# Kernel optimization log

Measured on AMD Instinct MI355X. Metric: run time of the kernel, lower is better.

Reference implementation:

```python
import jax, jax.numpy as jnp
import numpy as np

NUM_HEADS = 8
QUERY_DIM = 512
VALUE_DIM = 512
INPUT_DIM = 512
Q_HEAD = QUERY_DIM // NUM_HEADS   # 64
V_HEAD = VALUE_DIM // NUM_HEADS   # 64
TOPK = 5
BN_EPS = 1e-5


def setup_inputs() -> dict:
    key = jax.random.key(0)
    ks = jax.random.split(key, 3)
    B = 2048
    x = jax.random.normal(ks[0], (B, INPUT_DIM), dtype=jnp.float32)
    # small init scale so softmax logits are reasonable
    W_qkv = jax.random.normal(ks[1], (INPUT_DIM, 2 * QUERY_DIM + VALUE_DIM), dtype=jnp.float32) * 0.02
    W_proj = jax.random.normal(ks[2], (VALUE_DIM, VALUE_DIM), dtype=jnp.float32) * 0.02
    b_proj = jnp.zeros((VALUE_DIM,), dtype=jnp.float32)
    bn_gamma = jnp.ones((VALUE_DIM,), dtype=jnp.float32)
    bn_beta = jnp.zeros((VALUE_DIM,), dtype=jnp.float32)
    return {"x": x, "W_qkv": W_qkv, "W_proj": W_proj, "b_proj": b_proj,
            "bn_gamma": bn_gamma, "bn_beta": bn_beta}


def _batchnorm_train(y, gamma, beta):
    # torch BatchNorm1d training mode: batch mean, biased variance
    mean = y.mean(axis=0)
    var = y.var(axis=0)  # biased (ddof=0), matches torch normalization
    return gamma * (y - mean) * jax.lax.rsqrt(var + BN_EPS) + beta


def reference(x, W_qkv, W_proj, b_proj, bn_gamma, bn_beta):
    B = x.shape[0]
    # qkv_transform: Linear(input_dim, 2Q + V, bias=False)
    qkv = x @ W_qkv                                   # [B, 2Q+V]
    qv = qkv[:, :2 * QUERY_DIM].reshape(B, 2, NUM_HEADS, Q_HEAD)
    q = qv[:, 0].transpose(1, 0, 2)                   # [H, B, hd]
    k = qv[:, 1].transpose(1, 0, 2)                   # [H, B, hd]
    v = qkv[:, 2 * QUERY_DIM:].reshape(B, NUM_HEADS, V_HEAD).transpose(1, 0, 2)  # [H, B, vd]

    scale = 1.0 / jnp.sqrt(jnp.float32(Q_HEAD))
    logits = jnp.einsum('hqd,hkd->hqk', q, k) * scale  # [H, B, B]
    attn = jax.nn.softmax(logits, axis=-1)

    # per-head: zero the top-5 columns by summed attention weight (no grad through selection)
    col_sums = jax.lax.stop_gradient(attn.sum(axis=1))           # [H, B]
    _, top_idx = jax.lax.top_k(col_sums, TOPK)                   # [H, 5]
    mask = jnp.ones((NUM_HEADS, B), dtype=attn.dtype)
    mask = mask.at[jnp.arange(NUM_HEADS)[:, None], top_idx].set(0.0)
    attn = attn * mask[:, None, :]                               # zero columns

    out = jnp.einsum('hqk,hkd->hqd', attn, v)                    # [H, B, vd]
    out = out.transpose(1, 0, 2).reshape(B, VALUE_DIM)
    # proj: Linear + BatchNorm1d (training mode) + ReLU
    out = out @ W_proj.T + b_proj
    out = jax.nn.relu(_batchnorm_train(out, bn_gamma, bn_beta))
    return out, attn
```

## Files before the change

### kernel.cpp

```cpp
#include <hip/hip_runtime.h>
#include <hip/hip_bf16.h>

#define B 2048
#define NH 8
#define HD 64
#define DIM 512
#define QKVN 1536
#define OUT0_ELEMS ((size_t)B * DIM)

typedef float f32x4 __attribute__((ext_vector_type(4)));
typedef __bf16 bf16x8 __attribute__((ext_vector_type(8)));

static __device__ __forceinline__ unsigned short f2bf(float f) {
    unsigned int u = __builtin_bit_cast(unsigned int, f);
    u += 0x7fffu + ((u >> 16) & 1u);
    return (unsigned short)(u >> 16);
}
static __device__ __forceinline__ float bfhi2f(unsigned int u) {
    return __builtin_bit_cast(float, u & 0xffff0000u);
}
static __device__ __forceinline__ float bflo2f(unsigned int u) {
    return __builtin_bit_cast(float, u << 16);
}

__global__ __launch_bounds__(256) void prep_cast(const float* __restrict__ x,
                                                 const float* __restrict__ wp,
                                                 const float* __restrict__ wqkv,
                                                 unsigned short* __restrict__ xbf,
                                                 unsigned short* __restrict__ wpbf,
                                                 unsigned short* __restrict__ wT,
                                                 float* __restrict__ zero_region) {
    int bx = blockIdx.x;
    int tid = threadIdx.x;
    if (bx < 1280) {
        size_t t = (size_t)bx * 256 + tid;
        const float4* src;
        ushort4* dst;
        size_t idx;
        if (t < 262144) { src = (const float4*)x; dst = (ushort4*)xbf; idx = t; }
        else            { src = (const float4*)wp; dst = (ushort4*)wpbf; idx = t - 262144; }
        float4 v = src[idx];
        ushort4 u;
        u.x = f2bf(v.x); u.y = f2bf(v.y); u.z = f2bf(v.z); u.w = f2bf(v.w);
        dst[idx] = u;
        return;
    }
    if (bx >= 1472) {
        int idx = (bx - 1472) * 256 + tid;
        if (idx < 8448)
            ((float4*)zero_region)[idx] = make_float4(0.f, 0.f, 0.f, 0.f);
        return;
    }
    int b = bx - 1280;
    int n0 = (b % 24) * 64;
    int k0 = (b / 24) * 64;
    __shared__ unsigned short T[64][72];
#pragma unroll
    for (int it = 0; it < 4; ++it) {
        int chunk = it * 256 + tid;
        int r = chunk >> 4, c4 = (chunk & 15) * 4;
        float4 v = *(const float4*)(wqkv + (size_t)(k0 + r) * QKVN + n0 + c4);
        T[c4 + 0][r] = f2bf(v.x); T[c4 + 1][r] = f2bf(v.y);
        T[c4 + 2][r] = f2bf(v.z); T[c4 + 3][r] = f2bf(v.w);
    }
    __syncthreads();
#pragma unroll
    for (int it = 0; it < 2; ++it) {
        int chunk = it * 256 + tid;
        int r = chunk >> 3, c8 = (chunk & 7) * 8;
        ushort4 u0, u1;
        u0.x = T[r][c8 + 0]; u0.y = T[r][c8 + 1]; u0.z = T[r][c8 + 2]; u0.w = T[r][c8 + 3];
        u1.x = T[r][c8 + 4]; u1.y = T[r][c8 + 5]; u1.z = T[r][c8 + 6]; u1.w = T[r][c8 + 7];
        *(ushort4*)(wT + (size_t)(n0 + r) * 512 + k0 + c8) = u0;
        *(ushort4*)(wT + (size_t)(n0 + r) * 512 + k0 + c8 + 4) = u1;
    }
}

__global__ __launch_bounds__(256) void gemm_qkv_mfma(const unsigned short* __restrict__ xbf,
                                                     const unsigned short* __restrict__ wT,
                                                     float* __restrict__ v_f32,
                                                     unsigned short* __restrict__ qkbf,
                                                     unsigned short* __restrict__ vT) {
    int nt = blockIdx.x;
    int mt = blockIdx.y;
    __shared__ uint4 Ax[128 * 8];
    __shared__ uint4 Bw[64 * 8];
    int tid = threadIdx.x;
    int l = tid & 63, wid = tid >> 6;
    int wr = wid >> 1, wc = wid & 1;
    const uint4* x4 = (const uint4*)xbf;
    const uint4* w4 = (const uint4*)wT;
    f32x4 acc[4][2];
#pragma unroll
    for (int i = 0; i < 4; ++i)
#pragma unroll
        for (int j = 0; j < 2; ++j) acc[i][j] = (f32x4){0.f, 0.f, 0.f, 0.f};

    for (int kt = 0; kt < 8; ++kt) {
        int kg = kt * 8;
#pragma unroll
        for (int it = 0; it < 4; ++it) {
            int chunk = it * 256 + tid;
            int row = chunk >> 3, slot = chunk & 7;
            Ax[row * 8 + (slot ^ (row & 7))] = x4[(size_t)(mt * 128 + row) * 64 + kg + slot];
        }
#pragma unroll
        for (int it = 0; it < 2; ++it) {
            int chunk = it * 256 + tid;
            int row = chunk >> 3, slot = chunk & 7;
            Bw[row * 8 + (slot ^ (row & 7))] = w4[(size_t)(nt * 64 + row) * 64 + kg + slot];
        }
        __syncthreads();
#pragma unroll
        for (int km = 0; km < 2; ++km) {
            int gsel = km * 4 + (l >> 4);
            bf16x8 a[4], b[2];
#pragma unroll
            for (int i = 0; i < 4; ++i) {
                int row = wr * 64 + i * 16 + (l & 15);
                a[i] = __builtin_bit_cast(bf16x8, Ax[row * 8 + (gsel ^ (row & 7))]);
            }
#pragma unroll
            for (int j = 0; j < 2; ++j) {
                int row = wc * 32 + j * 16 + (l & 15);
                b[j] = __builtin_bit_cast(bf16x8, Bw[row * 8 + (gsel ^ (row & 7))]);
            }
#pragma unroll
            for (int i = 0; i < 4; ++i)
#pragma unroll
                for (int j = 0; j < 2; ++j)
                    acc[i][j] = __builtin_amdgcn_mfma_f32_16x16x32_bf16(a[i], b[j], acc[i][j], 0, 0, 0);
        }
        __syncthreads();
    }
    if (nt < 16) {
        float qscale = (nt < 8) ? 0.125f : 1.0f;
#pragma unroll
        for (int i = 0; i < 4; ++i)
#pragma unroll
            for (int j = 0; j < 2; ++j)
#pragma unroll
                for (int reg = 0; reg < 4; ++reg) {
                    int row = mt * 128 + wr * 64 + i * 16 + (l >> 4) * 4 + reg;
                    int col = nt * 64 + wc * 32 + j * 16 + (l & 15);
                    qkbf[(size_t)row * 1024 + col] = f2bf(acc[i][j][reg] * qscale);
                }
    } else {
        int h = nt - 16;
#pragma unroll
        for (int i = 0; i < 4; ++i)
#pragma unroll
            for (int j = 0; j < 2; ++j) {
                int k0r = mt * 128 + wr * 64 + i * 16 + (l >> 4) * 4;
                int d = wc * 32 + j * 16 + (l & 15);
                uint2 pk;
                pk.x = (unsigned)f2bf(acc[i][j][0]) | ((unsigned)f2bf(acc[i][j][1]) << 16);
                pk.y = (unsigned)f2bf(acc[i][j][2]) | ((unsigned)f2bf(acc[i][j][3]) << 16);
                *(uint2*)(vT + ((size_t)(h * 64 + d) * 2048 + k0r)) = pk;
#pragma unroll
                for (int reg = 0; reg < 4; ++reg)
                    v_f32[(size_t)(k0r + reg) * DIM + h * 64 + d] = acc[i][j][reg];
            }
    }
}

template<int PHASE>
__global__ __launch_bounds__(256) void attn_pass(const unsigned short* __restrict__ qkbf,
                                                 const unsigned short* __restrict__ vT,
                                                 const float* __restrict__ rowsum_in,
                                                 float* __restrict__ rowsum_out,
                                                 float* __restrict__ attn,
                                                 float* __restrict__ colsum,
                                                 float* __restrict__ ovp) {
    int ct = blockIdx.x, qt = blockIdx.y, h = blockIdx.z;
    int tid = threadIdx.x;
    int l = tid & 63;
    int wid = tid >> 6;
    int wr = wid >> 1;
    int wc = wid & 1;

    __shared__ uint4 Qs[128 * 8];
    __shared__ uint4 Ks[64 * 8];
    __shared__ uint4 Vt[64 * 8];
    __shared__ uint4 Pl4[128 * 8];
    __shared__ float cs[512];
    __shared__ float rinv[128];
    unsigned short* Pl = (unsigned short*)Pl4;

    const uint4* src = (const uint4*)qkbf;
#pragma unroll
    for (int it = 0; it < 4; ++it) {
        int chunk = it * 256 + tid;
        int row = chunk >> 3, slot = chunk & 7;
        Qs[row * 8 + (slot ^ (row & 7))] = src[(size_t)(qt * 128 + row) * 128 + h * 8 + slot];
    }
    if constexpr (PHASE == 2) {
        if (tid < 128) rinv[tid] = 1.0f / rowsum_in[h * B + qt * 128 + tid];
        if (tid < 256) { cs[tid] = 0.f; cs[tid + 256] = 0.f; }
    }

    float rsum[4][4];
    f32x4 O[4][2];
    if constexpr (PHASE == 1) {
#pragma unroll
        for (int i = 0; i < 4; ++i)
#pragma unroll
            for (int r = 0; r < 4; ++r) rsum[i][r] = 0.f;
    } else {
#pragma unroll
        for (int i = 0; i < 4; ++i)
#pragma unroll
            for (int j = 0; j < 2; ++j) O[i][j] = (f32x4){0.f, 0.f, 0.f, 0.f};
    }

    size_t hbb = (size_t)h * B * B;
    for (int sub = 0; sub < 8; ++sub) {
        int kbase = ct * 512 + sub * 64;
#pragma unroll
        for (int it = 0; it < 2; ++it) {
            int chunk = it * 256 + tid;
            int row = chunk >> 3, slot = chunk & 7;
            Ks[row * 8 + (slot ^ (row & 7))] = src[(size_t)(kbase + row) * 128 + 64 + h * 8 + slot];
        }
        if constexpr (PHASE == 2) {
#pragma unroll
            for (int it = 0; it < 2; ++it) {
                int chunk = it * 256 + tid;
                int d = chunk >> 3, g = chunk & 7;
                Vt[d * 8 + (g ^ (d & 7))] =
                    *(const uint4*)(vT + ((size_t)(h * 64 + d) * 2048 + kbase + g * 8));
            }
        }
        __syncthreads();

        f32x4 S[4][2];
#pragma unroll
        for (int i = 0; i < 4; ++i)
#pragma unroll
            for (int j = 0; j < 2; ++j) S[i][j] = (f32x4){0.f, 0.f, 0.f, 0.f};
#pragma unroll
        for (int km = 0; km < 2; ++km) {
            int gsel = km * 4 + (l >> 4);
            bf16x8 aq[4], bk[2];
#pragma unroll
            for (int i = 0; i < 4; ++i) {
                int row = wr * 64 + i * 16 + (l & 15);
                aq[i] = __builtin_bit_cast(bf16x8, Qs[row * 8 + (gsel ^ (row & 7))]);
            }
#pragma unroll
            for (int j = 0; j < 2; ++j) {
                int row = wc * 32 + j * 16 + (l & 15);
                bk[j] = __builtin_bit_cast(bf16x8, Ks[row * 8 + (gsel ^ (row & 7))]);
            }
#pragma unroll
            for (int i = 0; i < 4; ++i)
#pragma unroll
                for (int j = 0; j < 2; ++j)
                    S[i][j] = __builtin_amdgcn_mfma_f32_16x16x32_bf16(aq[i], bk[j], S[i][j], 0, 0, 0);
        }

        if constexpr (PHASE == 1) {
#pragma unroll
            for (int i = 0; i < 4; ++i)
#pragma unroll
                for (int j = 0; j < 2; ++j)
#pragma unroll
                    for (int reg = 0; reg < 4; ++reg)
                        rsum[i][reg] += __expf(S[i][j][reg]);
            __syncthreads();
        } else {
            float csacc[2] = {0.f, 0.f};
#pragma unroll
            for (int i = 0; i < 4; ++i) {
#pragma unroll
                for (int j = 0; j < 2; ++j) {
                    int kcol = wc * 32 + j * 16 + (l & 15);
#pragma unroll
                    for (int reg = 0; reg < 4; ++reg) {
                        int qrow = wr * 64 + i * 16 + (l >> 4) * 4 + reg;
                        float p = __expf(S[i][j][reg]) * rinv[qrow];
                        csacc[j] += p;
                        Pl[qrow * 64 + ((kcol & 7) | ((((kcol >> 3) ^ (qrow & 7))) << 3))] = f2bf(p);
                    }
                }
            }
#pragma unroll
            for (int j = 0; j < 2; ++j) {
                float v = csacc[j];
                v += __shfl_xor(v, 16);
                v += __shfl_xor(v, 32);
                if (l < 16) atomicAdd(&cs[sub * 64 + wc * 32 + j * 16 + l], v);
            }
            __syncthreads();
#pragma unroll
            for (int it2 = 0; it2 < 4; ++it2) {
                int chunk = it2 * 256 + tid;
                int row = chunk >> 3, g = chunk & 7;
                uint4 pv = Pl4[row * 8 + (g ^ (row & 7))];
                float4 lo, hi;
                lo.x = bflo2f(pv.x); lo.y = bfhi2f(pv.x);
                lo.z = bflo2f(pv.y); lo.w = bfhi2f(pv.y);
                hi.x = bflo2f(pv.z); hi.y = bfhi2f(pv.z);
                hi.z = bflo2f(pv.w); hi.w = bfhi2f(pv.w);
                float* dst = attn + hbb + (size_t)(qt * 128 + row) * B + kbase + g * 8;
                *(float4*)dst = lo;
                *(float4*)(dst + 4) = hi;
            }
#pragma unroll
            for (int km = 0; km < 2; ++km) {
                int gsel = km * 4 + (l >> 4);
                bf16x8 pa[4], vb[2];
#pragma unroll
                for (int i = 0; i < 4; ++i) {
                    int q = wr * 64 + i * 16 + (l & 15);
                    pa[i] = __builtin_bit_cast(bf16x8, Pl4[q * 8 + (gsel ^ (q & 7))]);
                }
#pragma unroll
                for (int j = 0; j < 2; ++j) {
                    int d = wc * 32 + j * 16 + (l & 15);
                    vb[j] = __builtin_bit_cast(bf16x8, Vt[d * 8 + (gsel ^ (d & 7))]);
                }
#pragma unroll
                for (int i = 0; i < 4; ++i)
#pragma unroll
                    for (int j = 0; j < 2; ++j)
                        O[i][j] = __builtin_amdgcn_mfma_f32_16x16x32_bf16(pa[i], vb[j], O[i][j], 0, 0, 0);
            }
            __syncthreads();
        }
    }

    if constexpr (PHASE == 1) {
#pragma unroll
        for (int i = 0; i < 4; ++i)
#pragma unroll
            for (int reg = 0; reg < 4; ++reg) {
                float v = rsum[i][reg];
                v += __shfl_xor(v, 1); v += __shfl_xor(v, 2);
                v += __shfl_xor(v, 4); v += __shfl_xor(v, 8);
                if ((l & 15) == 0)
                    atomicAdd(&rowsum_out[h * B + qt * 128 + wr * 64 + i * 16 + (l >> 4) * 4 + reg], v);
            }
    } else {
        for (int i = tid; i < 512; i += 256)
            atomicAdd(&colsum[h * B + ct * 512 + i], cs[i]);
#pragma unroll
        for (int i = 0; i < 4; ++i)
#pragma unroll
            for (int j = 0; j < 2; ++j)
#pragma unroll
                for (int reg = 0; reg < 4; ++reg) {
                    int qrow = wr * 64 + i * 16 + (l >> 4) * 4 + reg;
                    ovp[((size_t)ct * B + qt * 128 + qrow) * DIM + h * 64 + wc * 32 + j * 16 + (l & 15)] =
                        O[i][j][reg];
                }
    }
}

__global__ __launch_bounds__(256) void maskfix_topk(float* __restrict__ attn,
                                                    const float* __restrict__ v_f32,
                                                    const float* __restrict__ colsum,
                                                    const float* __restrict__ ovp,
                                                    unsigned short* __restrict__ ovbf) {
    int rt = blockIdx.x;
    int h = blockIdx.y;
    int tid = threadIdx.x;
    __shared__ float v[B];
    __shared__ float bv[256];
    __shared__ int bi[256];
    __shared__ float Pl[5][64];
    __shared__ float Vl[5][64];
    __shared__ int tix[5];
    for (int i = tid; i < B; i += 256) v[i] = colsum[h * B + i];
    __syncthreads();
    for (int it = 0; it < 5; ++it) {
        float best = -1e30f;
        int bidx = 0;
        for (int i = tid; i < B; i += 256) {
            float x = v[i];
            if (x > best || (x == best && i < bidx)) { best = x; bidx = i; }
        }
        bv[tid] = best; bi[tid] = bidx;
        __syncthreads();
        for (int s = 128; s > 0; s >>= 1) {
            if (tid < s) {
                if (bv[tid + s] > bv[tid] ||
                    (bv[tid + s] == bv[tid] && bi[tid + s] < bi[tid])) {
                    bv[tid] = bv[tid + s]; bi[tid] = bi[tid + s];
                }
            }
            __syncthreads();
        }
        if (tid == 0) { tix[it] = bi[0]; v[bi[0]] = -1e30f; }
        __syncthreads();
    }
    size_t abase = (size_t)h * B * B + (size_t)(rt * 64) * B;
    for (int t = tid; t < 320; t += 256) {
        int i = t / 64, q = t % 64;
        Pl[i][q] = attn[abase + (size_t)q * B + tix[i]];
        Vl[i][q] = v_f32[(size_t)tix[i] * DIM + h * 64 + q];
    }
    __syncthreads();
    for (int t = tid; t < 320; t += 256) {
        int i = t / 64, q = t % 64;
        attn[abase + (size_t)q * B + tix[i]] = 0.f;
    }
    int tx = tid % 16, ty = tid / 16;
    float corr[4][4] = {};
#pragma unroll
    for (int i = 0; i < 5; ++i)
#pragma unroll
        for (int a = 0; a < 4; ++a)
#pragma unroll
            for (int b2 = 0; b2 < 4; ++b2)
                corr[a][b2] += Pl[i][ty * 4 + a] * Vl[i][tx * 4 + b2];
#pragma unroll
    for (int a = 0; a < 4; ++a) {
        size_t row = (size_t)(rt * 64 + ty * 4 + a);
        size_t col = h * 64 + tx * 4;
        float4 s0 = *(const float4*)(ovp + ((size_t)0 * B + row) * DIM + col);
        float4 s1 = *(const float4*)(ovp + ((size_t)1 * B + row) * DIM + col);
        float4 s2 = *(const float4*)(ovp + ((size_t)2 * B + row) * DIM + col);
        float4 s3 = *(const float4*)(ovp + ((size_t)3 * B + row) * DIM + col);
        ushort4 u;
        u.x = f2bf(s0.x + s1.x + s2.x + s3.x - corr[a][0]);
        u.y = f2bf(s0.y + s1.y + s2.y + s3.y - corr[a][1]);
        u.z = f2bf(s0.z + s1.z + s2.z + s3.z - corr[a][2]);
        u.w = f2bf(s0.w + s1.w + s2.w + s3.w - corr[a][3]);
        *(ushort4*)(ovbf + row * DIM + col) = u;
    }
}

__global__ __launch_bounds__(256) void proj_gemm_mfma(const unsigned short* __restrict__ ovbf,
                                                      const unsigned short* __restrict__ wpbf,
                                                      const float* __restrict__ bproj,
                                                      float* __restrict__ y,
                                                      float* __restrict__ sums,
                                                      float* __restrict__ ssums) {
    int nt = blockIdx.x;
    int mt = blockIdx.y;
    __shared__ uint4 Ax[128 * 8];
    __shared__ uint4 Bw[64 * 8];
    __shared__ float sb[64];
    __shared__ float qb[64];
    int tid = threadIdx.x;
    int l = tid & 63, wid = tid >> 6;
    int wr = wid >> 1, wc = wid & 1;
    if (tid < 64) { sb[tid] = 0.f; qb[tid] = 0.f; }
    const uint4* a4 = (const uint4*)ovbf;
    const uint4* b4 = (const uint4*)wpbf;
    f32x4 acc[4][2];
#pragma unroll
    for (int i = 0; i < 4; ++i)
#pragma unroll
        for (int j = 0; j < 2; ++j) acc[i][j] = (f32x4){0.f, 0.f, 0.f, 0.f};

    for (int kt = 0; kt < 8; ++kt) {
        int kg = kt * 8;
#pragma unroll
        for (int it = 0; it < 4; ++it) {
            int chunk = it * 256 + tid;
            int row = chunk >> 3, slot = chunk & 7;
            Ax[row * 8 + (slot ^ (row & 7))] = a4[(size_t)(mt * 128 + row) * 64 + kg + slot];
        }
#pragma unroll
        for (int it = 0; it < 2; ++it) {
            int chunk = it * 256 + tid;
            int row = chunk >> 3, slot = chunk & 7;
            Bw[row * 8 + (slot ^ (row & 7))] = b4[(size_t)(nt * 64 + row) * 64 + kg + slot];
        }
        __syncthreads();
#pragma unroll
        for (int km = 0; km < 2; ++km) {
            int gsel = km * 4 + (l >> 4);
            bf16x8 a[4], b[2];
#pragma unroll
            for (int i = 0; i < 4; ++i) {
                int row = wr * 64 + i * 16 + (l & 15);
                a[i] = __builtin_bit_cast(bf16x8, Ax[row * 8 + (gsel ^ (row & 7))]);
            }
#pragma unroll
            for (int j = 0; j < 2; ++j) {
                int row = wc * 32 + j * 16 + (l & 15);
                b[j] = __builtin_bit_cast(bf16x8, Bw[row * 8 + (gsel ^ (row & 7))]);
            }
#pragma unroll
            for (int i = 0; i < 4; ++i)
#pragma unroll
                for (int j = 0; j < 2; ++j)
                    acc[i][j] = __builtin_amdgcn_mfma_f32_16x16x32_bf16(a[i], b[j], acc[i][j], 0, 0, 0);
        }
        __syncthreads();
    }
    float ls[2] = {0.f, 0.f};
    float lq[2] = {0.f, 0.f};
#pragma unroll
    for (int i = 0; i < 4; ++i)
#pragma unroll
        for (int j = 0; j < 2; ++j) {
            int col = nt * 64 + wc * 32 + j * 16 + (l & 15);
            float bp = bproj[col];
#pragma unroll
            for (int reg = 0; reg < 4; ++reg) {
                int row = mt * 128 + wr * 64 + i * 16 + (l >> 4) * 4 + reg;
                float c = acc[i][j][reg] + bp;
                y[(size_t)row * DIM + col] = c;
                ls[j] += c; lq[j] += c * c;
            }
        }
#pragma unroll
    for (int j = 0; j < 2; ++j) {
        atomicAdd(&sb[wc * 32 + j * 16 + (l & 15)], ls[j]);
        atomicAdd(&qb[wc * 32 + j * 16 + (l & 15)], lq[j]);
    }
    __syncthreads();
    if (tid < 64) {
        atomicAdd(&sums[nt * 64 + tid], sb[tid]);
        atomicAdd(&ssums[nt * 64 + tid], qb[tid]);
    }
}

__global__ __launch_bounds__(256) void bn_apply(const float* __restrict__ y,
                                                const float* __restrict__ sums,
                                                const float* __restrict__ ssums,
                                                const float* __restrict__ gamma,
                                                const float* __restrict__ beta,
                                                float* __restrict__ out) {
    int t = blockIdx.x * 256 + threadIdx.x;
    int c4 = (t % 128) * 4;
    size_t r = t / 128;
    if (r >= B) return;
    float4 s = *(const float4*)(sums + c4);
    float4 q = *(const float4*)(ssums + c4);
    float4 m, rs;
    m.x = s.x * (1.0f / B); m.y = s.y * (1.0f / B);
    m.z = s.z * (1.0f / B); m.w = s.w * (1.0f / B);
    rs.x = rsqrtf(q.x * (1.0f / B) - m.x * m.x + 1e-5f);
    rs.y = rsqrtf(q.y * (1.0f / B) - m.y * m.y + 1e-5f);
    rs.z = rsqrtf(q.z * (1.0f / B) - m.z * m.z + 1e-5f);
    rs.w = rsqrtf(q.w * (1.0f / B) - m.w * m.w + 1e-5f);
    float4 v = *(const float4*)(y + r * DIM + c4);
    float4 g = *(const float4*)(gamma + c4);
    float4 bt = *(const float4*)(beta + c4);
    float4 o;
    o.x = fmaxf(0.f, g.x * (v.x - m.x) * rs.x + bt.x);
    o.y = fmaxf(0.f, g.y * (v.y - m.y) * rs.y + bt.y);
    o.z = fmaxf(0.f, g.z * (v.z - m.z) * rs.z + bt.z);
    o.w = fmaxf(0.f, g.w * (v.w - m.w) * rs.w + bt.w);
    *(float4*)(out + r * DIM + c4) = o;
}

extern "C" void kernel_launch(void* const* d_in, const int* in_sizes, int n_in,
                              void* d_out, int out_size, void* d_ws, size_t ws_size,
                              hipStream_t stream) {
    const float* x = (const float*)d_in[0];
    const float* W_qkv = (const float*)d_in[1];
    const float* W_proj = (const float*)d_in[2];
    const float* b_proj = (const float*)d_in[3];
    const float* bn_gamma = (const float*)d_in[4];
    const float* bn_beta = (const float*)d_in[5];

    float* out0 = (float*)d_out;
    float* attn = (float*)d_out + OUT0_ELEMS;

    float* ws = (float*)d_ws;
    float* v_f32 = ws;
    float* ovp = v_f32 + OUT0_ELEMS;
    float* y = ovp + 4 * OUT0_ELEMS;
    float* rowsum = y + OUT0_ELEMS;
    float* colsum = rowsum + NH * B;
    float* sums = colsum + NH * B;
    float* ssums = sums + DIM;
    unsigned short* qkbf = (unsigned short*)(ssums + DIM);
    unsigned short* vT = qkbf + (size_t)B * 1024;
    unsigned short* wpbf = vT + (size_t)NH * HD * B;
    unsigned short* ovbf = wpbf + (size_t)DIM * DIM;
    unsigned short* xbf = (unsigned short*)ovp;
    unsigned short* wT = xbf + (size_t)B * 512;

    prep_cast<<<1280 + 192 + 33, 256, 0, stream>>>(x, W_proj, W_qkv, xbf, wpbf, wT, rowsum);
    gemm_qkv_mfma<<<dim3(QKVN / 64, B / 128), 256, 0, stream>>>(xbf, wT, v_f32, qkbf, vT);
    attn_pass<1><<<dim3(4, 16, NH), 256, 0, stream>>>(qkbf, vT, nullptr, rowsum,
                                                      attn, colsum, ovp);
    attn_pass<2><<<dim3(4, 16, NH), 256, 0, stream>>>(qkbf, vT, rowsum, nullptr,
                                                      attn, colsum, ovp);
    maskfix_topk<<<dim3(B / 64, NH), 256, 0, stream>>>(attn, v_f32, colsum, ovp, ovbf);
    proj_gemm_mfma<<<dim3(DIM / 64, B / 128), 256, 0, stream>>>(ovbf, wpbf, b_proj,
                                                                y, sums, ssums);
    bn_apply<<<(B * DIM / 4 + 255) / 256, 256, 0, stream>>>(y, sums, ssums,
                                                            bn_gamma, bn_beta, out0);
}
```

Measured before the change: 99.64 us.

## Fuse projection GEMM with batchnorm apply via grid-wide atomic barrier

Merges the projection GEMM and the batchnorm+ReLU kernel into one launch. All 128 blocks spin on a global atomic counter until every block has added its column sums, then normalize straight from the accumulator registers. This drops the y intermediate's write and re-read and one launch. It relies on all 128 blocks being co-resident, and the spin loop has a bounded timeout that could give wrong results if that does not hold.

```diff
diff --git a/kernel.cpp b/kernel.cpp
--- a/kernel.cpp
+++ b/kernel.cpp
@@ -47,7 +47,7 @@
     }
     if (bx >= 1472) {
         int idx = (bx - 1472) * 256 + tid;
-        if (idx < 8448)
+        if (idx < 8449)
             ((float4*)zero_region)[idx] = make_float4(0.f, 0.f, 0.f, 0.f);
         return;
     }
@@ -431,12 +431,15 @@
     }
 }
 
-__global__ __launch_bounds__(256) void proj_gemm_mfma(const unsigned short* __restrict__ ovbf,
-                                                      const unsigned short* __restrict__ wpbf,
-                                                      const float* __restrict__ bproj,
-                                                      float* __restrict__ y,
-                                                      float* __restrict__ sums,
-                                                      float* __restrict__ ssums) {
+__global__ __launch_bounds__(256) void proj_bn_fused(const unsigned short* __restrict__ ovbf,
+                                                     const unsigned short* __restrict__ wpbf,
+                                                     const float* __restrict__ bproj,
+                                                     const float* __restrict__ gamma,
+                                                     const float* __restrict__ beta,
+                                                     float* __restrict__ sums,
+                                                     float* __restrict__ ssums,
+                                                     int* __restrict__ ctr,
+                                                     float* __restrict__ out0) {
     int nt = blockIdx.x;
     int mt = blockIdx.y;
     __shared__ uint4 Ax[128 * 8];
@@ -495,19 +498,18 @@
     float ls[2] = {0.f, 0.f};
     float lq[2] = {0.f, 0.f};
 #pragma unroll
-    for (int i = 0; i < 4; ++i)
-#pragma unroll
-        for (int j = 0; j < 2; ++j) {
-            int col = nt * 64 + wc * 32 + j * 16 + (l & 15);
-            float bp = bproj[col];
+    for (int j = 0; j < 2; ++j) {
+        int col = nt * 64 + wc * 32 + j * 16 + (l & 15);
+        float bp = bproj[col];
+#pragma unroll
+        for (int i = 0; i < 4; ++i)
 #pragma unroll
             for (int reg = 0; reg < 4; ++reg) {
-                int row = mt * 128 + wr * 64 + i * 16 + (l >> 4) * 4 + reg;
                 float c = acc[i][j][reg] + bp;
-                y[(size_t)row * DIM + col] = c;
+                acc[i][j][reg] = c;
                 ls[j] += c; lq[j] += c * c;
             }
-        }
+    }
 #pragma unroll
     for (int j = 0; j < 2; ++j) {
         atomicAdd(&sb[wc * 32 + j * 16 + (l & 15)], ls[j]);
@@ -517,37 +519,47 @@
     if (tid < 64) {
         atomicAdd(&sums[nt * 64 + tid], sb[tid]);
         atomicAdd(&ssums[nt * 64 + tid], qb[tid]);
-    }
-}
-
-__global__ __launch_bounds__(256) void bn_apply(const float* __restrict__ y,
-                                                const float* __restrict__ sums,
-                                                const float* __restrict__ ssums,
-                                                const float* __restrict__ gamma,
-                                                const float* __restrict__ beta,
-                                                float* __restrict__ out) {
-    int t = blockIdx.x * 256 + threadIdx.x;
-    int c4 = (t % 128) * 4;
-    size_t r = t / 128;
-    if (r >= B) return;
-    float4 s = *(const float4*)(sums + c4);
-    float4 q = *(const float4*)(ssums + c4);
-    float4 m, rs;
-    m.x = s.x * (1.0f / B); m.y = s.y * (1.0f / B);
-    m.z = s.z * (1.0f / B); m.w = s.w * (1.0f / B);
-    rs.x = rsqrtf(q.x * (1.0f / B) - m.x * m.x + 1e-5f);
-    rs.y = rsqrtf(q.y * (1.0f / B) - m.y * m.y + 1e-5f);
-    rs.z = rsqrtf(q.z * (1.0f / B) - m.z * m.z + 1e-5f);
-    rs.w = rsqrtf(q.w * (1.0f / B) - m.w * m.w + 1e-5f);
-    float4 v = *(const float4*)(y + r * DIM + c4);
-    float4 g = *(const float4*)(gamma + c4);
-    float4 bt = *(const float4*)(beta + c4);
-    float4 o;
-    o.x = fmaxf(0.f, g.x * (v.x - m.x) * rs.x + bt.x);
-    o.y = fmaxf(0.f, g.y * (v.y - m.y) * rs.y + bt.y);
-    o.z = fmaxf(0.f, g.z * (v.z - m.z) * rs.z + bt.z);
-    o.w = fmaxf(0.f, g.w * (v.w - m.w) * rs.w + bt.w);
-    *(float4*)(out + r * DIM + c4) = o;
+        __threadfence();
+    }
+    __syncthreads();
+
+    if (tid == 0) {
+        atomicAdd(ctr, 1);
+        int spins = 0;
+        while (atomicAdd(ctr, 0) < 128 && spins < (1 << 20)) {
+            ++spins;
+            __builtin_amdgcn_s_sleep(2);
+        }
+    }
+    __syncthreads();
+    __threadfence();
+
+    if (tid < 64) {
+        float sv = atomicAdd(&sums[nt * 64 + tid], 0.0f);
+        float qv = atomicAdd(&ssums[nt * 64 + tid], 0.0f);
+        float m = sv * (1.0f / B);
+        sb[tid] = m;
+        qb[tid] = rsqrtf(qv * (1.0f / B) - m * m + 1e-5f);
+    }
+    __syncthreads();
+
+#pragma unroll
+    for (int j = 0; j < 2; ++j) {
+        int cl = wc * 32 + j * 16 + (l & 15);
+        int col = nt * 64 + cl;
+        float m = sb[cl];
+        float rs = qb[cl];
+        float g = gamma[col];
+        float bt = beta[col];
+#pragma unroll
+        for (int i = 0; i < 4; ++i)
+#pragma unroll
+            for (int reg = 0; reg < 4; ++reg) {
+                int row = mt * 128 + wr * 64 + i * 16 + (l >> 4) * 4 + reg;
+                out0[(size_t)row * DIM + col] =
+                    fmaxf(0.f, g * (acc[i][j][reg] - m) * rs + bt);
+            }
+    }
 }
 
 extern "C" void kernel_launch(void* const* d_in, const int* in_sizes, int n_in,
@@ -571,22 +583,22 @@
     float* colsum = rowsum + NH * B;
     float* sums = colsum + NH * B;
     float* ssums = sums + DIM;
-    unsigned short* qkbf = (unsigned short*)(ssums + DIM);
+    int* ctr = (int*)(ssums + DIM);
+    unsigned short* qkbf = (unsigned short*)(ssums + DIM + 4);
     unsigned short* vT = qkbf + (size_t)B * 1024;
     unsigned short* wpbf = vT + (size_t)NH * HD * B;
     unsigned short* ovbf = wpbf + (size_t)DIM * DIM;
     unsigned short* xbf = (unsigned short*)ovp;
     unsigned short* wT = xbf + (size_t)B * 512;
 
-    prep_cast<<<1280 + 192 + 33, 256, 0, stream>>>(x, W_proj, W_qkv, xbf, wpbf, wT, rowsum);
+    prep_cast<<<1280 + 192 + 34, 256, 0, stream>>>(x, W_proj, W_qkv, xbf, wpbf, wT, rowsum);
     gemm_qkv_mfma<<<dim3(QKVN / 64, B / 128), 256, 0, stream>>>(xbf, wT, v_f32, qkbf, vT);
     attn_pass<1><<<dim3(4, 16, NH), 256, 0, stream>>>(qkbf, vT, nullptr, rowsum,
                                                       attn, colsum, ovp);
     attn_pass<2><<<dim3(4, 16, NH), 256, 0, stream>>>(qkbf, vT, rowsum, nullptr,
                                                       attn, colsum, ovp);
     maskfix_topk<<<dim3(B / 64, NH), 256, 0, stream>>>(attn, v_f32, colsum, ovp, ovbf);
-    proj_gemm_mfma<<<dim3(DIM / 64, B / 128), 256, 0, stream>>>(ovbf, wpbf, b_proj,
-                                                                y, sums, ssums);
-    bn_apply<<<(B * DIM / 4 + 255) / 256, 256, 0, stream>>>(y, sums, ssums,
-                                                            bn_gamma, bn_beta, out0);
-}
+    proj_bn_fused<<<dim3(DIM / 64, B / 128), 256, 0, stream>>>(ovbf, wpbf, b_proj,
+                                                               bn_gamma, bn_beta,
+                                                               sums, ssums, ctr, out0);
+}
```

Measured after the change: 110.3 us. 1.11x slower.
